# Optimization experiments

Hardware: AMD Instinct MI355X
Metric: run time of the kernel (lower is better)

## Reference

```python
import jax, jax.numpy as jnp
import numpy as np

K = 4
TEMPERATURE = 34.0
OUT_CH = 256
KSIZE = 3
PAD = 1


def setup_inputs() -> dict:
    key = jax.random.key(0)
    ks = jax.random.split(key, 6)
    B, C, H, W = 16, 256, 56, 56
    hidden = int(C * 0.25) + 1  # 65
    x = jax.random.normal(ks[0], (B, C, H, W), dtype=jnp.float32)
    w_fc1 = jax.random.normal(ks[1], (hidden, C), dtype=jnp.float32) * (2.0 / C) ** 0.5
    w_fc2 = jax.random.normal(ks[2], (K, hidden), dtype=jnp.float32) * (2.0 / hidden) ** 0.5
    b_fc2 = jnp.zeros((K,), dtype=jnp.float32)
    weight = jax.random.normal(ks[3], (OUT_CH, C, KSIZE, KSIZE), dtype=jnp.float32) * 0.05
    bias = jax.random.normal(ks[4], (K, OUT_CH), dtype=jnp.float32) * 0.01
    return {"x": x, "w_fc1": w_fc1, "w_fc2": w_fc2, "b_fc2": b_fc2,
            "weight": weight, "bias": bias}


def _attention(x, w_fc1, w_fc2, b_fc2):
    pooled = x.mean(axis=(2, 3))                     # [B, C] adaptive avgpool(1)
    h = jax.nn.relu(pooled @ w_fc1.T)                # 1x1 conv == linear
    raw = h @ w_fc2.T + b_fc2                        # [B, K]
    # gradient_approximation: hard one-hot fwd, softmax(x/T) bwd (straight-through)
    hard = jax.nn.one_hot(jnp.argmax(raw, axis=1), raw.shape[1], dtype=raw.dtype)
    soft = jax.nn.softmax(raw / TEMPERATURE, axis=1)
    att = jax.lax.stop_gradient(hard - soft) + soft
    return att, raw


def _quantize_banks(weight):
    # WDoReFaQuantizer with 'modified' scheme, bits 2..K+1, STE on the round step
    w = weight.reshape(-1)
    t = jnp.tanh(w)
    xq = t / jnp.max(jnp.abs(t))
    xq = (xq + 1.0) * 0.5                            # in [0, 1]
    banks = []
    for bit in range(2, 2 + K):
        a = float(1 << bit)
        q = jnp.minimum(jnp.floor(a * xq), a - 1.0) / a
        q = jax.lax.stop_gradient(q - xq) + xq       # STE: identity backward
        banks.append(q * 2.0 - 1.0)
    return jnp.stack(banks)                          # [K, O*C*k*k]


def reference(x, w_fc1, w_fc2, b_fc2, weight, bias):
    B, C, H, W = x.shape
    att, raw = _attention(x, w_fc1, w_fc2, b_fc2)    # [B, K], [B, K]
    wq = _quantize_banks(weight)                     # [K, N]
    agg_w = (att @ wq).reshape(B, OUT_CH, C, KSIZE, KSIZE)
    agg_b = att @ bias                               # [B, OUT_CH]

    def conv1(xi, wi):  # xi: [C,H,W], wi: [O,C,k,k]
        return jax.lax.conv_general_dilated(
            xi[None], wi, window_strides=(1, 1),
            padding=[(PAD, PAD), (PAD, PAD)],
            dimension_numbers=("NCHW", "OIHW", "NCHW"))[0]

    out = jax.vmap(conv1)(x, agg_w) + agg_b[:, :, None, None]
    return (out, raw)
```

## Files before the change

kernel.cpp:

```cpp
#include <hip/hip_runtime.h>
#include <math.h>

#define NB 16
#define NC 256
#define NH 56
#define NW 56
#define NHW 3136
#define NHID 65
#define NK 4
#define NOC 256
#define WN 589824
#define OUT0 12845056

#define WS_POOLED 0
#define WS_KB     4096
#define WS_MAX    4112
#define WS_MAXP   4128
#define WS_WQF    8192
#define WQB_OFF   32768ul
#define XP_OFF    4751360ul
#define WS_NEED   32325632ul

typedef unsigned int u32;
typedef unsigned short u16;
typedef unsigned long long u64;
typedef __attribute__((ext_vector_type(8))) short s8v;
typedef __attribute__((ext_vector_type(16))) float f16v;

__device__ __forceinline__ u16 f2bf(float f) {
    union { float f; u32 u; } v; v.f = f;
    u32 u = v.u;
    return (u16)((u + 0x7fffu + ((u >> 16) & 1u)) >> 16);
}

__device__ __forceinline__ void gload_lds16(const void* g, void* l) {
    __builtin_amdgcn_global_load_lds((const __attribute__((address_space(1))) u32*)g,
                                     (__attribute__((address_space(3))) u32*)l, 16, 0, 0);
}


__global__ __launch_bounds__(256) void k_prep(const float* __restrict__ x,
                                              const float* __restrict__ w,
                                              float* __restrict__ ws,
                                              float* __restrict__ scratch) {
    const int tid = threadIdx.x;
    if (blockIdx.x >= 896) {
        int j = blockIdx.x - 896;
        float m = 0.f;
        for (int i = j * 256 + tid; i < WN; i += 65536)
            m = fmaxf(m, fabsf(tanhf(w[i])));
        for (int off = 32; off > 0; off >>= 1) m = fmaxf(m, __shfl_down(m, off, 64));
        __shared__ float part[4];
        int lane = tid & 63, wv = tid >> 6;
        if (lane == 0) part[wv] = m;
        __syncthreads();
        if (tid == 0)
            ws[WS_MAXP + j] = fmaxf(fmaxf(part[0], part[1]), fmaxf(part[2], part[3]));
        return;
    }
    const int by = blockIdx.x;
    const int b = by / 56, y = by % 56;
    const int c16 = tid >> 4, q = tid & 15;
    __shared__ __align__(8) u16 Lbt[56 * 264];
    __shared__ float pl[256];
    u16* xp = (u16*)((char*)ws + XP_OFF);

    #pragma unroll
    for (int ci = 0; ci < 16; ++ci) {
        int c = ci * 16 + c16;
        float4 v = make_float4(0.f, 0.f, 0.f, 0.f);
        if (q < 14) {
            v = *(const float4*)(x + ((size_t)(b * 256 + c)) * NHW + (size_t)y * 56 + q * 4);
            Lbt[(q * 4 + 0) * 264 + c] = f2bf(v.x);
            Lbt[(q * 4 + 1) * 264 + c] = f2bf(v.y);
            Lbt[(q * 4 + 2) * 264 + c] = f2bf(v.z);
            Lbt[(q * 4 + 3) * 264 + c] = f2bf(v.w);
        }
        float s = v.x + v.y + v.z + v.w;
        s += __shfl_down(s, 8, 16);
        s += __shfl_down(s, 4, 16);
        s += __shfl_down(s, 2, 16);
        s += __shfl_down(s, 1, 16);
        if (q == 0) pl[c] = s;
    }
    __syncthreads();
    scratch[(size_t)by * 256 + tid] = pl[tid];
    u64* rowp = (u64*)xp + (size_t)(b * 58 + y + 1) * (58 * 64);
    for (int idx = tid; idx < 58 * 64; idx += 256) {
        int col = idx >> 6, cp = idx & 63;
        u64 v = 0ull;
        if (col >= 1 && col <= 56)
            v = *(const u64*)(Lbt + (col - 1) * 264 + cp * 4);
        rowp[idx] = v;
    }
    if (y == 0 || y == 55) {
        int row = (y == 0) ? 0 : 57;
        u64* brow = (u64*)xp + (size_t)(b * 58 + row) * (58 * 64);
        for (int idx = tid; idx < 58 * 64; idx += 256) brow[idx] = 0ull;
    }
}

__global__ __launch_bounds__(256) void k_mid(const float* __restrict__ w_fc1,
                                             const float* __restrict__ w_fc2,
                                             const float* __restrict__ b_fc2,
                                             const float* __restrict__ w,
                                             float* __restrict__ ws,
                                             const float* __restrict__ scratch,
                                             float* __restrict__ out_raw) {
    const int tid = threadIdx.x;
    if (blockIdx.x < 16) {
        const int b = blockIdx.x;
        __shared__ float pl[NC];
        __shared__ float hs[NHID];
        __shared__ float raws[NK];
        float p = 0.f;
        for (int y = 0; y < 56; ++y)
            p += scratch[((size_t)(b * 56 + y)) * 256 + tid];
        pl[tid] = p * (1.0f / NHW);
        __syncthreads();
        if (tid < NHID) {
            float s = 0.f;
            for (int c = 0; c < NC; ++c) s = fmaf(pl[c], w_fc1[tid * NC + c], s);
            hs[tid] = fmaxf(s, 0.f);
        }
        __syncthreads();
        if (tid < NK) {
            float s = b_fc2[tid];
            for (int j = 0; j < NHID; ++j) s = fmaf(hs[j], w_fc2[tid * NHID + j], s);
            raws[tid] = s;
            out_raw[b * NK + tid] = s;
        }
        __syncthreads();
        if (tid == 0) {
            int best = 0;
            for (int k = 1; k < NK; ++k) if (raws[k] > raws[best]) best = k;
            ((int*)(ws + WS_KB))[b] = best;
        }
        return;
    }
    __shared__ float mred[4];
    float mv = ws[WS_MAXP + tid];
    for (int off = 32; off > 0; off >>= 1) mv = fmaxf(mv, __shfl_down(mv, off, 64));
    if ((tid & 63) == 0) mred[tid >> 6] = mv;
    __syncthreads();
    const float maxt = fmaxf(fmaxf(mred[0], mred[1]), fmaxf(mred[2], mred[3]));

    u16* wqp = (u16*)((char*)ws + WQB_OFF);
    int idx = (blockIdx.x - 16) * 256 + tid;
    int o = idx >> 7, c2 = idx & 127;
    int ch0 = c2 * 2;
    int cs = ch0 >> 5, cc = ch0 & 31;
    int ks2 = cc >> 4, hf = (cc >> 3) & 1, j = cc & 7;
    int n = o & 31, ot = o >> 5;
    const float* wp = w + ((size_t)o * 256 + ch0) * 9;
    float t0[9], t1[9];
    #pragma unroll
    for (int t = 0; t < 9; ++t) t0[t] = tanhf(wp[t]);
    #pragma unroll
    for (int t = 0; t < 9; ++t) t1[t] = tanhf(wp[9 + t]);
    #pragma unroll
    for (int bank = 0; bank < 4; ++bank) {
        float a = (float)(4 << bank);
        #pragma unroll
        for (int tap = 0; tap < 9; ++tap) {
            float xq0 = (t0[tap] / maxt + 1.f) * 0.5f;
            float xq1 = (t1[tap] / maxt + 1.f) * 0.5f;
            float q0 = fminf(floorf(a * xq0), a - 1.f) / a * 2.f - 1.f;
            float q1 = fminf(floorf(a * xq1), a - 1.f) / a * 2.f - 1.f;
            u32 pk = (u32)f2bf(q0) | ((u32)f2bf(q1) << 16);
            size_t off16 = ((((size_t)((bank * 8 + ot) * 8 + cs)) * 18 + tap * 2 + ks2) * 64
                            + hf * 32 + n) * 8 + j;
            *(u32*)(wqp + off16) = pk;
        }
    }
}

__global__ __launch_bounds__(256, 2) void k_conv_mfma(const float* __restrict__ bias,
                                                      const float* __restrict__ ws_f,
                                                      float* __restrict__ out) {
    const int oq = blockIdx.x;
    const int r0 = blockIdx.y * 8;
    const int b  = blockIdx.z;
    const int tid = threadIdx.x;
    const int wv = tid >> 6, lane = tid & 63;
    const int n = lane & 31, hf = lane >> 5;
    const int noff  = (wv < 2) ? wv * 4 : 8 + (wv - 2) * 3;
    const int ntile = (wv < 2) ? 4 : 3;
    const int kb = ((const int*)(ws_f + WS_KB))[b];
    const u16* wqp = (const u16*)((const char*)ws_f + WQB_OFF);
    const u16* xp  = (const u16*)((const char*)ws_f + XP_OFF);

    __shared__ __align__(16) u16 Xl[2][20480];

    int bofs[4];
    #pragma unroll
    for (int t = 0; t < 4; ++t) {
        int p = (noff + t) * 32 + n;
        if (t >= ntile) p = n;
        int pr = p / 56, pc = p - pr * 56;
        bofs[t] = pr * 4096 + hf * 1024 + pc * 16;
    }
    const int colc = (lane < 58) ? lane : 57;
    const u16* xsrc = xp + (((size_t)(b * 58 + r0)) * 58 + colc) * 256;
    const u16* ab0 = wqp + (size_t)((kb * 8 + oq * 2 + 0) * 8) * (18 * 64 * 8);
    const u16* ab1 = wqp + (size_t)((kb * 8 + oq * 2 + 1) * 8) * (18 * 64 * 8);

    f16v acc0[4], acc1[4];
    #pragma unroll
    for (int t = 0; t < 4; ++t) { acc0[t] = (f16v)0.f; acc1[t] = (f16v)0.f; }

    #pragma unroll
    for (int i = 0; i < 10; ++i) {
        int seg = wv * 10 + i;
        gload_lds16(xsrc + (size_t)(seg >> 2) * (58 * 256) + (seg & 3) * 8,
                    (void*)(&Xl[0][seg * 512]));
    }
    __syncthreads();

    #pragma unroll 1
    for (int cs = 0; cs < 8; ++cs) {
        int pb = cs & 1;
        if (cs < 7) {
            int c0n = (cs + 1) * 32;
            #pragma unroll
            for (int i = 0; i < 10; ++i) {
                int seg = wv * 10 + i;
                gload_lds16(xsrc + (size_t)(seg >> 2) * (58 * 256) + (seg & 3) * 8 + c0n,
                            (void*)(&Xl[pb ^ 1][seg * 512]));
            }
        }
        const u16* ap0 = ab0 + (size_t)cs * (18 * 64 * 8);
        const u16* ap1 = ab1 + (size_t)cs * (18 * 64 * 8);
        const char* XB = (const char*)&Xl[pb][0];
        #pragma unroll
        for (int r = 0; r < 3; ++r) {
            s8v a0[6], a1[6];
            #pragma unroll
            for (int j = 0; j < 6; ++j) {
                a0[j] = *(const s8v*)(ap0 + (size_t)((r * 6 + j) * 64 + lane) * 8);
                a1[j] = *(const s8v*)(ap1 + (size_t)((r * 6 + j) * 64 + lane) * 8);
            }
            #pragma unroll
            for (int s = 0; s < 3; ++s)
                #pragma unroll
                for (int ks = 0; ks < 2; ++ks) {
                    const int coff = r * 4096 + ks * 2048 + s * 16;
                    #pragma unroll
                    for (int t = 0; t < 4; ++t)
                        if (t < ntile) {
                            s8v bf = *(const s8v*)(XB + bofs[t] + coff);
                            acc0[t] = __builtin_amdgcn_mfma_f32_32x32x16_bf16(a0[s * 2 + ks], bf, acc0[t], 0, 0, 0);
                            acc1[t] = __builtin_amdgcn_mfma_f32_32x32x16_bf16(a1[s * 2 + ks], bf, acc1[t], 0, 0, 0);
                        }
                }
        }
        __syncthreads();
    }

    #pragma unroll
    for (int t = 0; t < 4; ++t)
        if (t < ntile) {
            int p = (noff + t) * 32 + n, pr = p / 56, pc = p - pr * 56;
            float* op = out + (size_t)b * 256 * NHW + (size_t)(r0 + pr) * 56 + pc;
            #pragma unroll
            for (int reg = 0; reg < 16; ++reg) {
                int m = (reg & 3) + 8 * (reg >> 2) + 4 * hf;
                int o0 = oq * 64 + m;
                op[(size_t)o0 * NHW] = acc0[t][reg] + bias[kb * NOC + o0];
                op[(size_t)(o0 + 32) * NHW] = acc1[t][reg] + bias[kb * NOC + o0 + 32];
            }
        }
}


__global__ __launch_bounds__(256) void k_pool(const float* __restrict__ x,
                                              float* __restrict__ ws) {
    int plane = blockIdx.x;
    const float* p = x + (size_t)plane * NHW;
    float s = 0.f;
    for (int i = threadIdx.x; i < NHW; i += 256) s += p[i];
    for (int off = 32; off > 0; off >>= 1) s += __shfl_down(s, off, 64);
    __shared__ float part[4];
    int lane = threadIdx.x & 63, wv = threadIdx.x >> 6;
    if (lane == 0) part[wv] = s;
    __syncthreads();
    if (threadIdx.x == 0)
        ws[WS_POOLED + plane] = part[0] + part[1] + part[2] + part[3];
}

__global__ __launch_bounds__(256) void k_fc(const float* __restrict__ w_fc1,
                                            const float* __restrict__ w_fc2,
                                            const float* __restrict__ b_fc2,
                                            float* __restrict__ ws,
                                            float* __restrict__ out_raw) {
    __shared__ float pl[NB * NC];
    __shared__ float hs[NB][NHID];
    __shared__ float raws[NB][NK];
    for (int i = threadIdx.x; i < NB * NC; i += 256)
        pl[i] = ws[WS_POOLED + i] * (1.0f / NHW);
    __syncthreads();
    for (int idx = threadIdx.x; idx < NB * NHID; idx += 256) {
        int b = idx / NHID, j = idx % NHID;
        float s = 0.f;
        for (int c = 0; c < NC; ++c) s = fmaf(pl[b * NC + c], w_fc1[j * NC + c], s);
        hs[b][j] = fmaxf(s, 0.f);
    }
    __syncthreads();
    if (threadIdx.x < NB * NK) {
        int b = threadIdx.x / NK, k = threadIdx.x % NK;
        float s = b_fc2[k];
        for (int j = 0; j < NHID; ++j) s = fmaf(hs[b][j], w_fc2[k * NHID + j], s);
        raws[b][k] = s;
        out_raw[b * NK + k] = s;
    }
    __syncthreads();
    if (threadIdx.x < NB) {
        int best = 0;
        for (int k = 1; k < NK; ++k)
            if (raws[threadIdx.x][k] > raws[threadIdx.x][best]) best = k;
        ((int*)(ws + WS_KB))[threadIdx.x] = best;
    }
}

__global__ __launch_bounds__(256) void k_maxtanh(const float* __restrict__ w,
                                                 float* __restrict__ ws) {
    float m = 0.f;
    for (int i = blockIdx.x * 256 + threadIdx.x; i < WN; i += gridDim.x * 256)
        m = fmaxf(m, fabsf(tanhf(w[i])));
    for (int off = 32; off > 0; off >>= 1) m = fmaxf(m, __shfl_down(m, off, 64));
    __shared__ float part[4];
    int lane = threadIdx.x & 63, wv = threadIdx.x >> 6;
    if (lane == 0) part[wv] = m;
    __syncthreads();
    if (threadIdx.x == 0) {
        float t = fmaxf(fmaxf(part[0], part[1]), fmaxf(part[2], part[3]));
        atomicMax((unsigned int*)ws + WS_MAX, __float_as_uint(t));
    }
}

__global__ __launch_bounds__(256) void k_quant(const float* __restrict__ w,
                                               float* __restrict__ ws) {
    float maxt = __uint_as_float(((const unsigned int*)ws)[WS_MAX]);
    float* wqf = ws + WS_WQF;
    for (int i = blockIdx.x * 256 + threadIdx.x; i < WN; i += gridDim.x * 256) {
        float t = tanhf(w[i]);
        float xq = (t / maxt + 1.0f) * 0.5f;
        #pragma unroll
        for (int k = 0; k < NK; ++k) {
            float a = (float)(4 << k);
            float q = fminf(floorf(a * xq), a - 1.0f) / a;
            wqf[(size_t)k * WN + i] = q * 2.0f - 1.0f;
        }
    }
}

__global__ __launch_bounds__(256) void k_conv(const float* __restrict__ x,
                                              const float* __restrict__ bias,
                                              const float* __restrict__ ws,
                                              float* __restrict__ out) {
    const int o_base = blockIdx.x * 16;
    const int row_base = blockIdx.y * 7;
    const int b = blockIdx.z;
    const int tid = threadIdx.x;
    const int w = tid & 63;
    const int og = tid >> 6;
    const int wc = (w < 56) ? w : 55;
    const int kb = ((const int*)(ws + WS_KB))[b];
    const float* wqf = ws + WS_WQF + (size_t)kb * WN;

    __shared__ float Xl[8][9][58];
    __shared__ float Wl[16][72];

    float acc[4][7];
    #pragma unroll
    for (int i = 0; i < 4; ++i)
        #pragma unroll
        for (int j = 0; j < 7; ++j) acc[i][j] = 0.f;

    for (int c0 = 0; c0 < NC; c0 += 8) {
        for (int idx = tid; idx < 1152; idx += 256) {
            int o = idx / 72, rem = idx - o * 72;
            Wl[o][rem] = wqf[(size_t)(o_base + o) * 2304 + c0 * 9 + rem];
        }
        for (int idx = tid; idx < 4176; idx += 256) {
            int c = idx / 522, rem = idx - c * 522;
            int ly = rem / 58, lx = rem - ly * 58;
            int gy = row_base - 1 + ly, gx = lx - 1;
            float v = 0.f;
            if (gy >= 0 && gy < NH && (unsigned)gx < (unsigned)NW)
                v = x[(((size_t)b * NC + c0 + c) * NH + gy) * NW + gx];
            Xl[c][ly][lx] = v;
        }
        __syncthreads();
        #pragma unroll 1
        for (int c = 0; c < 8; ++c) {
            float xv[9][3];
            #pragma unroll
            for (int ly = 0; ly < 9; ++ly)
                #pragma unroll
                for (int s = 0; s < 3; ++s)
                    xv[ly][s] = Xl[c][ly][wc + s];
            float wvv[4][9];
            #pragma unroll
            for (int i = 0; i < 4; ++i)
                #pragma unroll
                for (int t = 0; t < 9; ++t)
                    wvv[i][t] = Wl[og * 4 + i][c * 9 + t];
            #pragma unroll
            for (int i = 0; i < 4; ++i)
                #pragma unroll
                for (int j = 0; j < 7; ++j)
                    #pragma unroll
                    for (int r = 0; r < 3; ++r)
                        #pragma unroll
                        for (int s = 0; s < 3; ++s)
                            acc[i][j] = fmaf(wvv[i][r * 3 + s], xv[j + r][s], acc[i][j]);
        }
        __syncthreads();
    }

    if (w < 56) {
        #pragma unroll
        for (int i = 0; i < 4; ++i) {
            int o = o_base + og * 4 + i;
            float bb = bias[kb * NOC + o];
            #pragma unroll
            for (int j = 0; j < 7; ++j)
                out[(((size_t)b * NOC + o) * NH + (row_base + j)) * NW + w] = acc[i][j] + bb;
        }
    }
}

extern "C" void kernel_launch(void* const* d_in, const int* in_sizes, int n_in,
                              void* d_out, int out_size, void* d_ws, size_t ws_size,
                              hipStream_t stream) {
    const float* x      = (const float*)d_in[0];
    const float* w_fc1  = (const float*)d_in[1];
    const float* w_fc2  = (const float*)d_in[2];
    const float* b_fc2  = (const float*)d_in[3];
    const float* weight = (const float*)d_in[4];
    const float* bias   = (const float*)d_in[5];
    float* out = (float*)d_out;
    float* ws  = (float*)d_ws;

    if (ws_size >= WS_NEED) {
        hipLaunchKernelGGL(k_prep, dim3(1152), dim3(256), 0, stream, x, weight, ws, out);
        hipLaunchKernelGGL(k_mid, dim3(144), dim3(256), 0, stream,
                           w_fc1, w_fc2, b_fc2, weight, ws, out, out + OUT0);
        hipLaunchKernelGGL(k_conv_mfma, dim3(4, 7, 16), dim3(256), 0, stream, bias, ws, out);
    } else {
        hipLaunchKernelGGL(k_pool, dim3(NB * NC), dim3(256), 0, stream, x, ws);
        hipLaunchKernelGGL(k_fc, dim3(1), dim3(256), 0, stream,
                           w_fc1, w_fc2, b_fc2, ws, out + OUT0);
        hipLaunchKernelGGL(k_maxtanh, dim3(256), dim3(256), 0, stream, weight, ws);
        hipLaunchKernelGGL(k_quant, dim3(512), dim3(256), 0, stream, weight, ws);
        hipLaunchKernelGGL(k_conv, dim3(16, 8, NB), dim3(256), 0, stream, x, bias, ws, out);
    }
}
```

Before: 200.3 us.

## Retile conv into 512-block grid with XCD-aware mapping and 8-wave blocks

The MFMA conv kernel moves from a 3D grid of 448 blocks of 256 threads (8-row strips) to 512 blocks of 512 threads covering 7-row strips. Each wave now holds at most 2 pixel tiles instead of 4, and weight fragments are loaded per MFMA step rather than prefetched as 6 per row. Block indices are swizzled so that consecutive blocks on one XCD share batch/strip pairs, and the wave-to-tile assignment is rotated to balance uneven tiles. The goal is better occupancy, CU load balance and L2 locality, at the cost of more weight-fragment reloads per MFMA and smaller per-wave reuse.

```diff
diff --git a/kernel.cpp b/kernel.cpp
--- a/kernel.cpp
+++ b/kernel.cpp
@@ -175,28 +175,32 @@
     }
 }
 
-__global__ __launch_bounds__(256, 2) void k_conv_mfma(const float* __restrict__ bias,
+__global__ __launch_bounds__(512, 4) void k_conv_mfma(const float* __restrict__ bias,
                                                       const float* __restrict__ ws_f,
                                                       float* __restrict__ out) {
-    const int oq = blockIdx.x;
-    const int r0 = blockIdx.y * 8;
-    const int b  = blockIdx.z;
+    const int L = blockIdx.x;
+    const int xcd = L & 7, slot = L >> 3;
+    const int oq = slot >> 4;
+    const int pair = xcd * 16 + (slot & 15);
+    const int b = pair >> 3, strip = pair & 7;
+    const int r0 = strip * 7;
     const int tid = threadIdx.x;
     const int wv = tid >> 6, lane = tid & 63;
     const int n = lane & 31, hf = lane >> 5;
-    const int noff  = (wv < 2) ? wv * 4 : 8 + (wv - 2) * 3;
-    const int ntile = (wv < 2) ? 4 : 3;
+    const int vw = (wv + (slot & 7)) & 7;
+    const int ntile = (vw < 5) ? 2 : 1;
+    const int t0 = (vw < 5) ? vw * 2 : 10 + (vw - 5);
     const int kb = ((const int*)(ws_f + WS_KB))[b];
     const u16* wqp = (const u16*)((const char*)ws_f + WQB_OFF);
     const u16* xp  = (const u16*)((const char*)ws_f + XP_OFF);
 
-    __shared__ __align__(16) u16 Xl[2][20480];
-
-    int bofs[4];
-    #pragma unroll
-    for (int t = 0; t < 4; ++t) {
-        int p = (noff + t) * 32 + n;
-        if (t >= ntile) p = n;
+    __shared__ __align__(16) u16 Xl[2][18432];
+
+    int bofs[2];
+    #pragma unroll
+    for (int t = 0; t < 2; ++t) {
+        int p = (t0 + t) * 32 + n;
+        if (t >= ntile || p > 391) p = 391;
         int pr = p / 56, pc = p - pr * 56;
         bofs[t] = pr * 4096 + hf * 1024 + pc * 16;
     }
@@ -205,16 +209,19 @@
     const u16* ab0 = wqp + (size_t)((kb * 8 + oq * 2 + 0) * 8) * (18 * 64 * 8);
     const u16* ab1 = wqp + (size_t)((kb * 8 + oq * 2 + 1) * 8) * (18 * 64 * 8);
 
-    f16v acc0[4], acc1[4];
-    #pragma unroll
-    for (int t = 0; t < 4; ++t) { acc0[t] = (f16v)0.f; acc1[t] = (f16v)0.f; }
-
-    #pragma unroll
-    for (int i = 0; i < 10; ++i) {
-        int seg = wv * 10 + i;
-        gload_lds16(xsrc + (size_t)(seg >> 2) * (58 * 256) + (seg & 3) * 8,
-                    (void*)(&Xl[0][seg * 512]));
-    }
+    f16v acc0[2], acc1[2];
+    #pragma unroll
+    for (int t = 0; t < 2; ++t) { acc0[t] = (f16v)0.f; acc1[t] = (f16v)0.f; }
+
+    const int sbase = (wv < 4) ? wv * 5 : 20 + (wv - 4) * 4;
+    const int scnt  = (wv < 4) ? 5 : 4;
+    #pragma unroll
+    for (int i = 0; i < 5; ++i)
+        if (i < scnt) {
+            int seg = sbase + i;
+            gload_lds16(xsrc + (size_t)(seg >> 2) * (58 * 256) + (seg & 3) * 8,
+                        (void*)(&Xl[0][seg * 512]));
+        }
     __syncthreads();
 
     #pragma unroll 1
@@ -223,51 +230,51 @@
         if (cs < 7) {
             int c0n = (cs + 1) * 32;
             #pragma unroll
-            for (int i = 0; i < 10; ++i) {
-                int seg = wv * 10 + i;
-                gload_lds16(xsrc + (size_t)(seg >> 2) * (58 * 256) + (seg & 3) * 8 + c0n,
-                            (void*)(&Xl[pb ^ 1][seg * 512]));
-            }
+            for (int i = 0; i < 5; ++i)
+                if (i < scnt) {
+                    int seg = sbase + i;
+                    gload_lds16(xsrc + (size_t)(seg >> 2) * (58 * 256) + (seg & 3) * 8 + c0n,
+                                (void*)(&Xl[pb ^ 1][seg * 512]));
+                }
         }
         const u16* ap0 = ab0 + (size_t)cs * (18 * 64 * 8);
         const u16* ap1 = ab1 + (size_t)cs * (18 * 64 * 8);
         const char* XB = (const char*)&Xl[pb][0];
         #pragma unroll
-        for (int r = 0; r < 3; ++r) {
-            s8v a0[6], a1[6];
-            #pragma unroll
-            for (int j = 0; j < 6; ++j) {
-                a0[j] = *(const s8v*)(ap0 + (size_t)((r * 6 + j) * 64 + lane) * 8);
-                a1[j] = *(const s8v*)(ap1 + (size_t)((r * 6 + j) * 64 + lane) * 8);
-            }
+        for (int r = 0; r < 3; ++r)
             #pragma unroll
             for (int s = 0; s < 3; ++s)
                 #pragma unroll
                 for (int ks = 0; ks < 2; ++ks) {
+                    const int f = r * 6 + s * 2 + ks;
+                    s8v a0 = *(const s8v*)(ap0 + (size_t)(f * 64 + lane) * 8);
+                    s8v a1 = *(const s8v*)(ap1 + (size_t)(f * 64 + lane) * 8);
                     const int coff = r * 4096 + ks * 2048 + s * 16;
                     #pragma unroll
-                    for (int t = 0; t < 4; ++t)
+                    for (int t = 0; t < 2; ++t)
                         if (t < ntile) {
                             s8v bf = *(const s8v*)(XB + bofs[t] + coff);
-                            acc0[t] = __builtin_amdgcn_mfma_f32_32x32x16_bf16(a0[s * 2 + ks], bf, acc0[t], 0, 0, 0);
-                            acc1[t] = __builtin_amdgcn_mfma_f32_32x32x16_bf16(a1[s * 2 + ks], bf, acc1[t], 0, 0, 0);
+                            acc0[t] = __builtin_amdgcn_mfma_f32_32x32x16_bf16(a0, bf, acc0[t], 0, 0, 0);
+                            acc1[t] = __builtin_amdgcn_mfma_f32_32x32x16_bf16(a1, bf, acc1[t], 0, 0, 0);
                         }
                 }
-        }
-        __syncthreads();
-    }
-
-    #pragma unroll
-    for (int t = 0; t < 4; ++t)
+        __syncthreads();
+    }
+
+    #pragma unroll
+    for (int t = 0; t < 2; ++t)
         if (t < ntile) {
-            int p = (noff + t) * 32 + n, pr = p / 56, pc = p - pr * 56;
-            float* op = out + (size_t)b * 256 * NHW + (size_t)(r0 + pr) * 56 + pc;
-            #pragma unroll
-            for (int reg = 0; reg < 16; ++reg) {
-                int m = (reg & 3) + 8 * (reg >> 2) + 4 * hf;
-                int o0 = oq * 64 + m;
-                op[(size_t)o0 * NHW] = acc0[t][reg] + bias[kb * NOC + o0];
-                op[(size_t)(o0 + 32) * NHW] = acc1[t][reg] + bias[kb * NOC + o0 + 32];
+            int p = (t0 + t) * 32 + n;
+            if (p < 392) {
+                int pr = p / 56, pc = p - pr * 56;
+                float* op = out + (size_t)b * 256 * NHW + (size_t)(r0 + pr) * 56 + pc;
+                #pragma unroll
+                for (int reg = 0; reg < 16; ++reg) {
+                    int m = (reg & 3) + 8 * (reg >> 2) + 4 * hf;
+                    int o0 = oq * 64 + m;
+                    op[(size_t)o0 * NHW] = acc0[t][reg] + bias[kb * NOC + o0];
+                    op[(size_t)(o0 + 32) * NHW] = acc1[t][reg] + bias[kb * NOC + o0 + 32];
+                }
             }
         }
 }
@@ -447,7 +454,7 @@
         hipLaunchKernelGGL(k_prep, dim3(1152), dim3(256), 0, stream, x, weight, ws, out);
         hipLaunchKernelGGL(k_mid, dim3(144), dim3(256), 0, stream,
                            w_fc1, w_fc2, b_fc2, weight, ws, out, out + OUT0);
-        hipLaunchKernelGGL(k_conv_mfma, dim3(4, 7, 16), dim3(256), 0, stream, bias, ws, out);
+        hipLaunchKernelGGL(k_conv_mfma, dim3(512), dim3(512), 0, stream, bias, ws, out);
     } else {
         hipLaunchKernelGGL(k_pool, dim3(NB * NC), dim3(256), 0, stream, x, ws);
         hipLaunchKernelGGL(k_fc, dim3(1), dim3(256), 0, stream,
```

New measurement: 207.4 us. 1.04x slower.
